# Kernel optimization log

Measured on AMD Instinct MI355X. Metric: run time of the kernel, lower is better.

## Reference

```python
import jax, jax.numpy as jnp
import numpy as np

HDR_H, HDR_W = 16, 32  # HDR_map_shape[:2]


def _light_dirs_and_coeff():
    # Matl: unit direction per HDR texel, matching the torch double loop.
    phi = (jnp.arange(HDR_H, dtype=jnp.float32) / HDR_H) * jnp.pi          # (16,)
    theta = (jnp.arange(HDR_W, dtype=jnp.float32) / HDR_W) * (2 * jnp.pi)  # (32,)
    sp, cp = jnp.sin(phi)[:, None], jnp.cos(phi)[:, None]                  # (16,1)
    st, ct = jnp.sin(theta)[None, :], jnp.cos(theta)[None, :]              # (1,32)
    dirs = jnp.stack([st * sp, jnp.broadcast_to(cp, (HDR_H, HDR_W)), -ct * sp], axis=-1)  # (16,32,3)
    dirs = dirs / jnp.linalg.norm(dirs, axis=-1, keepdims=True)
    Matl = dirs.reshape(-1, 3).T                                            # (3, M=512)
    coeff = jnp.broadcast_to(sp[:, :, None], (HDR_H, 1, 3))                 # (16,1,3), sin(phi) per row
    return Matl, coeff


def setup_inputs() -> dict:
    key = jax.random.key(0)
    k1, k2, k3 = jax.random.split(key, 3)
    B, H, W = 2, 512, 512
    env = jax.random.uniform(k1, (B, HDR_H, HDR_W, 3), dtype=jnp.float32)
    normal = jax.random.uniform(k2, (B, H, W, 3), dtype=jnp.float32)
    albedo = jax.random.uniform(k3, (B, 3, H, W), dtype=jnp.float32)
    return {"env": env, "normal": normal, "albedo": albedo}


def reference(env, normal, albedo):
    B, H, W, _ = normal.shape
    Matl, coeff = _light_dirs_and_coeff()
    # HDR weighting: env * sin(phi) row coefficient -> (B, M, 3)
    hdr = (env * coeff[None]).reshape(B, HDR_H * HDR_W, 3)
    # Normal map: flip channel order (::-1) then decode to [-1,1]
    n = (normal[..., ::-1] - 0.5) * 2.0
    Matn = n.reshape(B, H * W, 3)                                           # (B, N, 3)
    # relu-clamped dot products against all light directions: (B, N, M)
    Matd = jax.nn.relu(jnp.einsum('bnk,km->bnm', Matn, Matl))
    # weight by HDR and reduce over light directions (same math as the per-channel torch loop)
    light = jnp.einsum('bnm,bmc->bnc', Matd, hdr)                           # (B, N, 3)
    lightmap = light.reshape(B, H, W, 3).transpose(0, 3, 1, 2)              # (B, 3, H, W)
    diffuse = (lightmap / 50.0) * albedo
    return diffuse
```

## Files before the change

kernel.cpp:

```cpp
#include <hip/hip_runtime.h>


constexpr int HW     = 512 * 512;
constexpr int WAVES  = 4;
constexpr int GROUPS = 16;

typedef _Float16 half2v __attribute__((ext_vector_type(2)));
typedef _Float16 half8  __attribute__((ext_vector_type(8)));
typedef float    f32x4  __attribute__((ext_vector_type(4)));

__device__ constexpr float SPc[8] = {
    0.195090322f, 0.382683432f, 0.555570233f, 0.707106781f,
    0.831469612f, 0.923879533f, 0.980785280f, 1.0f };
__device__ constexpr float CPc[8] = {
    0.980785280f, 0.923879533f, 0.831469612f, 0.707106781f,
    0.555570233f, 0.382683432f, 0.195090322f, 0.0f };
__device__ constexpr float STc[32] = {
    0.0f,          0.195090322f,  0.382683432f,  0.555570233f,
    0.707106781f,  0.831469612f,  0.923879533f,  0.980785280f,
    1.0f,          0.980785280f,  0.923879533f,  0.831469612f,
    0.707106781f,  0.555570233f,  0.382683432f,  0.195090322f,
    0.0f,         -0.195090322f, -0.382683432f, -0.555570233f,
   -0.707106781f, -0.831469612f, -0.923879533f, -0.980785280f,
   -1.0f,         -0.980785280f, -0.923879533f, -0.831469612f,
   -0.707106781f, -0.555570233f, -0.382683432f, -0.195090322f };
__device__ constexpr float CTc[32] = {
    1.0f,          0.980785280f,  0.923879533f,  0.831469612f,
    0.707106781f,  0.555570233f,  0.382683432f,  0.195090322f,
    0.0f,         -0.195090322f, -0.382683432f, -0.555570233f,
   -0.707106781f, -0.831469612f, -0.923879533f, -0.980785280f,
   -1.0f,         -0.980785280f, -0.923879533f, -0.831469612f,
   -0.707106781f, -0.555570233f, -0.382683432f, -0.195090322f,
    0.0f,          0.195090322f,  0.382683432f,  0.555570233f,
    0.707106781f,  0.923879533f,  0.923879533f,  0.980785280f };

union h8u { unsigned u[4]; half8 v; half2v h2[4]; };

__global__ __launch_bounds__(256, 4)
void env_render_fused(const float* __restrict__ env,
                      const float* __restrict__ normal,
                      const float* __restrict__ albedo,
                      float* __restrict__ out)
{
    __shared__ float lds_env[16 * 32 * 3];
    __shared__ half8 lds_hf[512];
    __shared__ float lds_nrm[WAVES][768];
    __shared__ float lds_light[WAVES][768];
    __shared__ float Wred[WAVES][9];

    const int b    = blockIdx.y;
    const int t    = threadIdx.x;
    const int lane = t & 63, wave = t >> 6;
    const int ch   = lane & 15, cg = lane >> 4;

    const int wavepx0 = (blockIdx.x * WAVES + wave) * (GROUPS * 16);

    #pragma unroll
    for (int q = 0; q < 6; ++q)
        lds_env[t + q * 256] = env[(size_t)b * 1536 + t + q * 256];

    {
        const float* nsrc = normal + ((size_t)b * HW + wavepx0) * 3;
        #pragma unroll
        for (int q = 0; q < 3; ++q) {
            const f32x4 v = *(const f32x4*)(nsrc + q * 256 + lane * 4);
            *(f32x4*)&lds_nrm[wave][q * 256 + lane * 4] = v;
        }
    }
    __syncthreads();

    #pragma unroll
    for (int ss = 0; ss < 2; ++ss) {
        const int s = t + ss * 256;
        const int tile = s >> 6, ln = s & 63;
        const int kc = ln >> 4, chh = ln & 15;
        const int j  = tile * 4 + kc;
        half8 f;
        #pragma unroll
        for (int e = 0; e < 8; ++e) {
            const int i = e + 1;
            float v = 0.f;
            if (chh < 3 && !(i == 8 && j >= 16)) {
                const int i2 = 16 - i, j2 = (j + 16) & 31;
                v = (lds_env[(i * 32 + j) * 3 + chh] +
                     lds_env[(i2 * 32 + j2) * 3 + chh]) * (SPc[e] * 0.01f);
            }
            f[e] = (_Float16)v;
        }
        lds_hf[s] = f;
    }

    float W[9];
    #pragma unroll
    for (int q = 0; q < 9; ++q) W[q] = 0.0f;
    if (t < 240) {
        int i, j;
        if (t < 224) { i = 1 + (t >> 5); j = t & 31; }
        else         { i = 8;            j = t - 224; }
        const int i2 = 16 - i, j2 = (j + 16) & 31;
        const float sp = SPc[i - 1], cp = CPc[i - 1];
        const int jm = j & 15;
        const float sbase = (jm == 0) ? 0.0f : ((jm <= 8) ? SPc[jm - 1] : CPc[jm - 9]);
        const float cbase = (jm == 0) ? 1.0f : ((jm <= 8) ? CPc[jm - 1] : -SPc[jm - 9]);
        const float st = (j < 16) ? sbase : -sbase;
        const float ct = (j < 16) ? cbase : -cbase;
        const float dx = st * sp, dy = cp, dz = -ct * sp;
        const float scale = sp * 0.01f;
        const float* ea = lds_env + (i * 32 + j) * 3;
        const float* eb = lds_env + (i2 * 32 + j2) * 3;
        const float hd0 = (ea[0] - eb[0]) * scale;
        const float hd1 = (ea[1] - eb[1]) * scale;
        const float hd2 = (ea[2] - eb[2]) * scale;
        W[0] = dx * hd0; W[1] = dx * hd1; W[2] = dx * hd2;
        W[3] = dy * hd0; W[4] = dy * hd1; W[5] = dy * hd2;
        W[6] = dz * hd0; W[7] = dz * hd1; W[8] = dz * hd2;
    }
    #pragma unroll
    for (int q = 0; q < 9; ++q) {
        float v = W[q];
        #pragma unroll
        for (int off = 32; off > 0; off >>= 1) v += __shfl_down(v, off);
        if (lane == 0) Wred[wave][q] = v;
    }
    __syncthreads();

    float Wl[9];
    #pragma unroll
    for (int q = 0; q < 9; ++q)
        Wl[q] = Wred[0][q] + Wred[1][q] + Wred[2][q] + Wred[3][q];

    half8 Hf[8];
    #pragma unroll
    for (int tl = 0; tl < 8; ++tl) Hf[tl] = lds_hf[tl * 64 + lane];

    half2v st2[4], ct2[4], sp2[4], cp2[4];
    #pragma unroll
    for (int p = 0; p < 4; ++p) {
        const int ja = (2 * p) * 4 + cg, jb = (2 * p + 1) * 4 + cg;
        st2[p] = half2v{(_Float16)STc[ja], (_Float16)STc[jb]};
        const float cta = ((ja + 8) & 31) < 16 ?  STc[(ja + 8) & 31] : STc[(ja + 8) & 31];
        const float ctb = ((jb + 8) & 31) < 16 ?  STc[(jb + 8) & 31] : STc[(jb + 8) & 31];
        ct2[p] = half2v{(_Float16)STc[(ja + 8) & 31], (_Float16)STc[(jb + 8) & 31]};
        (void)cta; (void)ctb;
        sp2[p] = half2v{(_Float16)SPc[2 * p], (_Float16)SPc[2 * p + 1]};
        cp2[p] = half2v{(_Float16)CPc[2 * p], (_Float16)CPc[2 * p + 1]};
    }

    #pragma unroll
    for (int g = 0; g < GROUPS; ++g) {
        const int pxl = g * 16 + ch;
        const float n0 = lds_nrm[wave][pxl * 3 + 0];
        const float n1 = lds_nrm[wave][pxl * 3 + 1];
        const float n2 = lds_nrm[wave][pxl * 3 + 2];

        const float nx = fmaf(n2, 2.0f, -1.0f);
        const float ny = fmaf(n1, 2.0f, -1.0f);
        const float nz = fmaf(n0, 2.0f, -1.0f);

        const _Float16 nxh = (_Float16)nx, nyh = (_Float16)ny, nzh = (_Float16)nz;
        const half2v nx2 = {nxh, nxh}, ny2 = {nyh, nyh}, nz2 = {nzh, nzh};

        half2v u2[4], nyc2[4];
        #pragma unroll
        for (int p = 0; p < 4; ++p) {
            u2[p]   = nx2 * st2[p] - nz2 * ct2[p];
            nyc2[p] = ny2 * cp2[p];
        }

        f32x4 acc = {0.f, 0.f, 0.f, 0.f};
        #pragma unroll
        for (int tl = 0; tl < 8; ++tl) {
            const _Float16 uh = (tl & 1) ? u2[tl >> 1].y : u2[tl >> 1].x;
            const half2v ub = {uh, uh};
            h8u pk;
            #pragma unroll
            for (int p = 0; p < 4; ++p) {
                const half2v d2 = sp2[p] * ub + nyc2[p];
                pk.h2[p] = d2;
                pk.u[p] &= 0x7FFF7FFFu;
            }
            acc = __builtin_amdgcn_mfma_f32_16x16x32_f16(Hf[tl], pk.v, acc, 0, 0, 0);
        }

        if (cg == 0) {
            lds_light[wave][pxl]       = acc[0] + fmaf(nx, Wl[0], fmaf(ny, Wl[3], nz * Wl[6]));
            lds_light[wave][256 + pxl] = acc[1] + fmaf(nx, Wl[1], fmaf(ny, Wl[4], nz * Wl[7]));
            lds_light[wave][512 + pxl] = acc[2] + fmaf(nx, Wl[2], fmaf(ny, Wl[5], nz * Wl[8]));
        }
    }
    __syncthreads();

    const size_t bbase = (size_t)b * 3 * HW + wavepx0;
    #pragma unroll
    for (int c = 0; c < 3; ++c) {
        const f32x4 av = *(const f32x4*)(albedo + bbase + (size_t)c * HW + lane * 4);
        const f32x4 lv = *(const f32x4*)&lds_light[wave][c * 256 + lane * 4];
        f32x4 ov;
        #pragma unroll
        for (int k = 0; k < 4; ++k) ov[k] = av[k] * lv[k];
        *(f32x4*)(out + bbase + (size_t)c * HW + lane * 4) = ov;
    }
}

extern "C" void kernel_launch(void* const* d_in, const int* in_sizes, int n_in,
                              void* d_out, int out_size, void* d_ws, size_t ws_size,
                              hipStream_t stream)
{
    const float* env    = (const float*)d_in[0];
    const float* normal = (const float*)d_in[1];
    const float* albedo = (const float*)d_in[2];
    float* out          = (float*)d_out;

    const int B = in_sizes[0] / (16 * 32 * 3);

    dim3 grid((HW / 16) / (WAVES * GROUPS), B);
    env_render_fused<<<grid, 256, 0, stream>>>(env, normal, albedo, out);
}
```

Measured before the change: 18.72 us.

## Split env preprocessing into setup kernel and shrink per-wave pixel tiles

Env-map preprocessing (fp16 HDR tiles and the 9-element linear correction) moves into a small per-batch setup kernel that writes to workspace. The main kernel then only copies the precomputed tiles into LDS, so each block no longer recomputes them redundantly. GROUPS drops from 16 to 4, giving four times as many blocks, with occupancy raised to 8 blocks per CU. The MFMA chain is split across two accumulators. The trade-offs are a second launch, scalar rather than vectorized albedo/output accesses, and a per-block LDS copy that is now amortized over fewer pixels.

```diff
diff --git a/kernel.cpp b/kernel.cpp
--- a/kernel.cpp
+++ b/kernel.cpp
@@ -3,7 +3,7 @@
 
 constexpr int HW     = 512 * 512;
 constexpr int WAVES  = 4;
-constexpr int GROUPS = 16;
+constexpr int GROUPS = 4;
 
 typedef _Float16 half2v __attribute__((ext_vector_type(2)));
 typedef _Float16 half8  __attribute__((ext_vector_type(8)));
@@ -24,49 +24,22 @@
    -0.707106781f, -0.831469612f, -0.923879533f, -0.980785280f,
    -1.0f,         -0.980785280f, -0.923879533f, -0.831469612f,
    -0.707106781f, -0.555570233f, -0.382683432f, -0.195090322f };
-__device__ constexpr float CTc[32] = {
-    1.0f,          0.980785280f,  0.923879533f,  0.831469612f,
-    0.707106781f,  0.555570233f,  0.382683432f,  0.195090322f,
-    0.0f,         -0.195090322f, -0.382683432f, -0.555570233f,
-   -0.707106781f, -0.831469612f, -0.923879533f, -0.980785280f,
-   -1.0f,         -0.980785280f, -0.923879533f, -0.831469612f,
-   -0.707106781f, -0.555570233f, -0.382683432f, -0.195090322f,
-    0.0f,          0.195090322f,  0.382683432f,  0.555570233f,
-    0.707106781f,  0.923879533f,  0.923879533f,  0.980785280f };
 
 union h8u { unsigned u[4]; half8 v; half2v h2[4]; };
 
-__global__ __launch_bounds__(256, 4)
-void env_render_fused(const float* __restrict__ env,
-                      const float* __restrict__ normal,
-                      const float* __restrict__ albedo,
-                      float* __restrict__ out)
+__global__ __launch_bounds__(256)
+void setup_kernel(const float* __restrict__ env,
+                  half8* __restrict__ hf_g,
+                  float* __restrict__ Wout)
 {
-    __shared__ float lds_env[16 * 32 * 3];
-    __shared__ half8 lds_hf[512];
-    __shared__ float lds_nrm[WAVES][768];
-    __shared__ float lds_light[WAVES][768];
-    __shared__ float Wred[WAVES][9];
-
-    const int b    = blockIdx.y;
-    const int t    = threadIdx.x;
+    __shared__ float lds_env[1536];
+    __shared__ float Wred[4][9];
+    const int b = blockIdx.x, t = threadIdx.x;
     const int lane = t & 63, wave = t >> 6;
-    const int ch   = lane & 15, cg = lane >> 4;
-
-    const int wavepx0 = (blockIdx.x * WAVES + wave) * (GROUPS * 16);
 
     #pragma unroll
     for (int q = 0; q < 6; ++q)
         lds_env[t + q * 256] = env[(size_t)b * 1536 + t + q * 256];
-
-    {
-        const float* nsrc = normal + ((size_t)b * HW + wavepx0) * 3;
-        #pragma unroll
-        for (int q = 0; q < 3; ++q) {
-            const f32x4 v = *(const f32x4*)(nsrc + q * 256 + lane * 4);
-            *(f32x4*)&lds_nrm[wave][q * 256 + lane * 4] = v;
-        }
-    }
     __syncthreads();
 
     #pragma unroll
@@ -87,7 +60,7 @@
             }
             f[e] = (_Float16)v;
         }
-        lds_hf[s] = f;
+        hf_g[b * 512 + s] = f;
     }
 
     float W[9];
@@ -99,11 +72,7 @@
         else         { i = 8;            j = t - 224; }
         const int i2 = 16 - i, j2 = (j + 16) & 31;
         const float sp = SPc[i - 1], cp = CPc[i - 1];
-        const int jm = j & 15;
-        const float sbase = (jm == 0) ? 0.0f : ((jm <= 8) ? SPc[jm - 1] : CPc[jm - 9]);
-        const float cbase = (jm == 0) ? 1.0f : ((jm <= 8) ? CPc[jm - 1] : -SPc[jm - 9]);
-        const float st = (j < 16) ? sbase : -sbase;
-        const float ct = (j < 16) ? cbase : -cbase;
+        const float st = STc[j], ct = STc[(j + 8) & 31];
         const float dx = st * sp, dy = cp, dz = -ct * sp;
         const float scale = sp * 0.01f;
         const float* ea = lds_env + (i * 32 + j) * 3;
@@ -123,28 +92,54 @@
         if (lane == 0) Wred[wave][q] = v;
     }
     __syncthreads();
+    if (t < 9) Wout[b * 9 + t] = Wred[0][t] + Wred[1][t] + Wred[2][t] + Wred[3][t];
+}
+
+__global__ __launch_bounds__(256, 8)
+void env_render_main(const float* __restrict__ normal,
+                     const float* __restrict__ albedo,
+                     const half8* __restrict__ hf_g,
+                     const float* __restrict__ Wm,
+                     float* __restrict__ out)
+{
+    __shared__ half8 lds_hf[512];
+    __shared__ float lds_nrm[WAVES][192];
+    __shared__ float lds_light[WAVES][192];
+
+    const int b    = blockIdx.y;
+    const int t    = threadIdx.x;
+    const int lane = t & 63, wave = t >> 6;
+    const int ch   = lane & 15, cg = lane >> 4;
+
+    {
+        const f32x4* src = (const f32x4*)(hf_g + (size_t)b * 512);
+        f32x4* dst = (f32x4*)lds_hf;
+        dst[t]       = src[t];
+        dst[t + 256] = src[t + 256];
+    }
+
+    const int wavepx0 = (blockIdx.x * WAVES + wave) * (GROUPS * 16);
+    {
+        const float* nsrc = normal + ((size_t)b * HW + wavepx0) * 3;
+        #pragma unroll
+        for (int q = 0; q < 3; ++q)
+            lds_nrm[wave][q * 64 + lane] = nsrc[q * 64 + lane];
+    }
 
     float Wl[9];
     #pragma unroll
-    for (int q = 0; q < 9; ++q)
-        Wl[q] = Wred[0][q] + Wred[1][q] + Wred[2][q] + Wred[3][q];
-
-    half8 Hf[8];
-    #pragma unroll
-    for (int tl = 0; tl < 8; ++tl) Hf[tl] = lds_hf[tl * 64 + lane];
+    for (int q = 0; q < 9; ++q) Wl[q] = Wm[b * 9 + q];
 
     half2v st2[4], ct2[4], sp2[4], cp2[4];
     #pragma unroll
     for (int p = 0; p < 4; ++p) {
         const int ja = (2 * p) * 4 + cg, jb = (2 * p + 1) * 4 + cg;
         st2[p] = half2v{(_Float16)STc[ja], (_Float16)STc[jb]};
-        const float cta = ((ja + 8) & 31) < 16 ?  STc[(ja + 8) & 31] : STc[(ja + 8) & 31];
-        const float ctb = ((jb + 8) & 31) < 16 ?  STc[(jb + 8) & 31] : STc[(jb + 8) & 31];
         ct2[p] = half2v{(_Float16)STc[(ja + 8) & 31], (_Float16)STc[(jb + 8) & 31]};
-        (void)cta; (void)ctb;
         sp2[p] = half2v{(_Float16)SPc[2 * p], (_Float16)SPc[2 * p + 1]};
         cp2[p] = half2v{(_Float16)CPc[2 * p], (_Float16)CPc[2 * p + 1]};
     }
+    __syncthreads();
 
     #pragma unroll
     for (int g = 0; g < GROUPS; ++g) {
@@ -152,7 +147,6 @@
         const float n0 = lds_nrm[wave][pxl * 3 + 0];
         const float n1 = lds_nrm[wave][pxl * 3 + 1];
         const float n2 = lds_nrm[wave][pxl * 3 + 2];
-
         const float nx = fmaf(n2, 2.0f, -1.0f);
         const float ny = fmaf(n1, 2.0f, -1.0f);
         const float nz = fmaf(n0, 2.0f, -1.0f);
@@ -167,7 +161,8 @@
             nyc2[p] = ny2 * cp2[p];
         }
 
-        f32x4 acc = {0.f, 0.f, 0.f, 0.f};
+        f32x4 acc0 = {0.f, 0.f, 0.f, 0.f};
+        f32x4 acc1 = {0.f, 0.f, 0.f, 0.f};
         #pragma unroll
         for (int tl = 0; tl < 8; ++tl) {
             const _Float16 uh = (tl & 1) ? u2[tl >> 1].y : u2[tl >> 1].x;
@@ -179,26 +174,25 @@
                 pk.h2[p] = d2;
                 pk.u[p] &= 0x7FFF7FFFu;
             }
-            acc = __builtin_amdgcn_mfma_f32_16x16x32_f16(Hf[tl], pk.v, acc, 0, 0, 0);
+            const half8 Hf = lds_hf[tl * 64 + lane];
+            if (tl < 4) acc0 = __builtin_amdgcn_mfma_f32_16x16x32_f16(Hf, pk.v, acc0, 0, 0, 0);
+            else        acc1 = __builtin_amdgcn_mfma_f32_16x16x32_f16(Hf, pk.v, acc1, 0, 0, 0);
         }
 
         if (cg == 0) {
-            lds_light[wave][pxl]       = acc[0] + fmaf(nx, Wl[0], fmaf(ny, Wl[3], nz * Wl[6]));
-            lds_light[wave][256 + pxl] = acc[1] + fmaf(nx, Wl[1], fmaf(ny, Wl[4], nz * Wl[7]));
-            lds_light[wave][512 + pxl] = acc[2] + fmaf(nx, Wl[2], fmaf(ny, Wl[5], nz * Wl[8]));
-        }
-    }
-    __syncthreads();
-
+            const float l0 = acc0[0] + acc1[0] + fmaf(nx, Wl[0], fmaf(ny, Wl[3], nz * Wl[6]));
+            const float l1 = acc0[1] + acc1[1] + fmaf(nx, Wl[1], fmaf(ny, Wl[4], nz * Wl[7]));
+            const float l2 = acc0[2] + acc1[2] + fmaf(nx, Wl[2], fmaf(ny, Wl[5], nz * Wl[8]));
+            lds_light[wave][pxl]       = l0;
+            lds_light[wave][64 + pxl]  = l1;
+            lds_light[wave][128 + pxl] = l2;
+        }
+    }
     const size_t bbase = (size_t)b * 3 * HW + wavepx0;
     #pragma unroll
     for (int c = 0; c < 3; ++c) {
-        const f32x4 av = *(const f32x4*)(albedo + bbase + (size_t)c * HW + lane * 4);
-        const f32x4 lv = *(const f32x4*)&lds_light[wave][c * 256 + lane * 4];
-        f32x4 ov;
-        #pragma unroll
-        for (int k = 0; k < 4; ++k) ov[k] = av[k] * lv[k];
-        *(f32x4*)(out + bbase + (size_t)c * HW + lane * 4) = ov;
+        const size_t o = bbase + (size_t)c * HW + lane;
+        out[o] = lds_light[wave][c * 64 + lane] * albedo[o];
     }
 }
 
@@ -210,9 +204,15 @@
     const float* normal = (const float*)d_in[1];
     const float* albedo = (const float*)d_in[2];
     float* out          = (float*)d_out;
+    char*  ws           = (char*)d_ws;
 
     const int B = in_sizes[0] / (16 * 32 * 3);
 
-    dim3 grid((HW / 16) / (WAVES * GROUPS), B);
-    env_render_fused<<<grid, 256, 0, stream>>>(env, normal, albedo, out);
+    half8* hf_g = (half8*)ws;
+    float* Wm   = (float*)(ws + (size_t)B * 512 * 16);
+
+    setup_kernel<<<dim3(B), 256, 0, stream>>>(env, hf_g, Wm);
+
+    dim3 grid(HW / (WAVES * GROUPS * 16), B);
+    env_render_main<<<grid, 256, 0, stream>>>(normal, albedo, hf_g, Wm, out);
 }
```

After: 21.02 us. +12.3%, slower.
